# Optimization experiments

Hardware: AMD Instinct MI355X
Metric: run time of the kernel (lower is better)

## Reference

```python
import jax, jax.numpy as jnp
import numpy as np

ALPHA = 1.0  # self.a buffer (alpha=1.0 default)


def setup_inputs() -> dict:
    key = jax.random.key(0)
    k1, k2, k3 = jax.random.split(key, 3)
    B, S, DIN, DOUT = 4, 2048, 4096, 4096
    # activations and weights are int8 in [-127, 127)
    x = jax.random.randint(k1, (B, S, DIN), -127, 127, dtype=jnp.int8)
    weight = jax.random.randint(k2, (DOUT, DIN), -127, 127, dtype=jnp.int8)
    bias = jax.random.normal(k3, (1, DOUT), dtype=jnp.float32)
    return {"x": x, "weight": weight, "bias": bias}


def reference(x, weight, bias):
    # x: [B, S, DIN] int8; weight: [DOUT, DIN] int8; bias: [1, DOUT] fp32
    x_shape = x.shape
    x2 = x.reshape(-1, x_shape[-1])  # [B*S, DIN]
    y = jnp.matmul(x2, weight.T, preferred_element_type=jnp.int32)  # [B*S, DOUT] int32
    # epilogue: y + round(bias / alpha); int32 + fp32 promotes to fp32 (matches torch)
    y = y.astype(jnp.float32) + jnp.round(bias / ALPHA)
    return y.reshape(*x_shape[:-1], y.shape[-1])
```

## Files before the change

kernel.cpp:

```cpp
#include <hip/hip_runtime.h>
#include <stdint.h>
#include <math.h>


typedef int i32x4 __attribute__((ext_vector_type(4)));

static constexpr int Mdim = 8192;
static constexpr int Ndim = 4096;
static constexpr int Kdim = 4096;
static constexpr int BM = 256;
static constexpr int BN = 256;
static constexpr int BKb = 128;
static constexpr int NKT = Kdim / BKb;
static constexpr int BUF_BYTES = 65536;

typedef const __attribute__((address_space(1))) unsigned int gu32;
typedef __attribute__((address_space(3))) unsigned int lu32;

__device__ __forceinline__ void gload_lds16(const int8_t* g, char* l) {
    __builtin_amdgcn_global_load_lds((gu32*)g, (lu32*)l, 16, 0, 0);
}

__global__ void pack_i32_to_i8_both(const int* __restrict__ X32,
                                    const int* __restrict__ W32,
                                    unsigned int* __restrict__ Xp,
                                    unsigned int* __restrict__ Wp,
                                    int nX4, int nT4) {
    int idx = blockIdx.x * blockDim.x + threadIdx.x;
    int stride = gridDim.x * blockDim.x;
    for (int i = idx; i < nT4; i += stride) {
        const int* src; unsigned int* dst; int j;
        if (i < nX4) { src = X32; dst = Xp; j = i; }
        else         { src = W32; dst = Wp; j = i - nX4; }
        i32x4 v = ((const i32x4*)src)[j];
        unsigned int o = ((unsigned)v[0] & 0xffu)
                       | (((unsigned)v[1] & 0xffu) << 8)
                       | (((unsigned)v[2] & 0xffu) << 16)
                       | (((unsigned)v[3]) << 24);
        dst[j] = o;
    }
}

__global__ __launch_bounds__(512, 2) void w8a8_gemm_256(
    const int8_t* __restrict__ X, const int8_t* __restrict__ Wt,
    const float* __restrict__ bias, float* __restrict__ out)
{
    __shared__ char smem[2 * BUF_BYTES];

    const int tid = threadIdx.x;
    const int w   = tid >> 6;
    const int l   = tid & 63;
    const int fr  = l & 15;
    const int fk  = l >> 4;
    const int wm  = w >> 2;
    const int wn  = w & 3;

    const int bm = blockIdx.x * BM;
    const int bn = blockIdx.y * BN;

    const int8_t* gA = X  + (size_t)(bm + l) * Kdim + w * 16;
    const int8_t* gB = Wt + (size_t)(bn + l) * Kdim + w * 16;
    const int ldsAw = w * 2048 + l * 16;
    const int ldsBw = 32768 + w * 2048 + l * 16;

    auto stageA = [&](int t, int hm) {
        const int bufo = (t & 1) * BUF_BYTES;
        const size_t ko = (size_t)t * BKb;
#pragma unroll
        for (int s = 0; s < 2; ++s)
            gload_lds16(gA + (size_t)(hm * 128 + s * 64) * Kdim + ko,
                        &smem[bufo + hm * 16384 + s * 1024 + ldsAw]);
    };
    auto stageB = [&](int t, int hn) {
        const int bufo = (t & 1) * BUF_BYTES;
        const size_t ko = (size_t)t * BKb;
#pragma unroll
        for (int s = 0; s < 2; ++s)
            gload_lds16(gB + (size_t)(hn * 128 + s * 64) * Kdim + ko,
                        &smem[bufo + hn * 16384 + s * 1024 + ldsBw]);
    };

    const int aBase = wm * 16384 + fk * 2048 + fr * 16;
    const int bBase = 32768 + (wn >> 1) * 16384 + fk * 2048
                    + ((wn & 1) * 64 + fr) * 16;

    i32x4 acc[8][4] = {};
    i32x4 a[4][2], b[4][2];

    stageB(0, 0); stageB(0, 1); stageA(0, 0); stageA(0, 1);
    stageB(1, 0); stageB(1, 1); stageA(1, 0); stageA(1, 1);
    asm volatile("s_waitcnt vmcnt(8)" ::: "memory");
    __syncthreads();

    for (int t = 0; t < NKT; ++t) {
        const int p = (t & 1) * BUF_BYTES;

#pragma unroll
        for (int ks = 0; ks < 2; ++ks) {
#pragma unroll
            for (int j = 0; j < 4; ++j)
                a[j][ks] = *(const i32x4*)&smem[p + aBase + ks * 8192 + j * 256];
#pragma unroll
            for (int ni = 0; ni < 2; ++ni)
                b[ni][ks] = *(const i32x4*)&smem[p + bBase + ks * 8192 + ni * 256];
        }
        __builtin_amdgcn_s_barrier();
        asm volatile("s_waitcnt lgkmcnt(0)" ::: "memory");
        __builtin_amdgcn_sched_barrier(0);
        __builtin_amdgcn_s_setprio(1);
#pragma unroll
        for (int ks = 0; ks < 2; ++ks)
#pragma unroll
            for (int j = 0; j < 4; ++j)
#pragma unroll
                for (int ni = 0; ni < 2; ++ni)
                    acc[j][ni] = __builtin_amdgcn_mfma_i32_16x16x64_i8(
                        a[j][ks], b[ni][ks], acc[j][ni], 0, 0, 0);
        __builtin_amdgcn_s_setprio(0);
        __builtin_amdgcn_s_barrier();

#pragma unroll
        for (int ks = 0; ks < 2; ++ks)
#pragma unroll
            for (int ni = 2; ni < 4; ++ni)
                b[ni][ks] = *(const i32x4*)&smem[p + bBase + ks * 8192 + ni * 256];
        __builtin_amdgcn_s_barrier();
        asm volatile("s_waitcnt lgkmcnt(0)" ::: "memory");
        __builtin_amdgcn_sched_barrier(0);
        __builtin_amdgcn_s_setprio(1);
#pragma unroll
        for (int ks = 0; ks < 2; ++ks)
#pragma unroll
            for (int j = 0; j < 4; ++j)
#pragma unroll
                for (int ni = 2; ni < 4; ++ni)
                    acc[j][ni] = __builtin_amdgcn_mfma_i32_16x16x64_i8(
                        a[j][ks], b[ni][ks], acc[j][ni], 0, 0, 0);
        __builtin_amdgcn_s_setprio(0);
        __builtin_amdgcn_s_barrier();

#pragma unroll
        for (int ks = 0; ks < 2; ++ks)
#pragma unroll
            for (int j = 0; j < 4; ++j)
                a[j][ks] = *(const i32x4*)&smem[p + aBase + ks * 8192 + 1024 + j * 256];
        if (t + 2 < NKT) { stageB(t + 2, 0); stageB(t + 2, 1); }
        __builtin_amdgcn_s_barrier();
        asm volatile("s_waitcnt lgkmcnt(0)" ::: "memory");
        __builtin_amdgcn_sched_barrier(0);
        __builtin_amdgcn_s_setprio(1);
#pragma unroll
        for (int ks = 0; ks < 2; ++ks)
#pragma unroll
            for (int j = 0; j < 4; ++j)
#pragma unroll
                for (int ni = 0; ni < 2; ++ni)
                    acc[4 + j][ni] = __builtin_amdgcn_mfma_i32_16x16x64_i8(
                        a[j][ks], b[ni][ks], acc[4 + j][ni], 0, 0, 0);
        __builtin_amdgcn_s_setprio(0);
        __builtin_amdgcn_s_barrier();

        if (t + 2 < NKT) { stageA(t + 2, 0); stageA(t + 2, 1); }
        __builtin_amdgcn_sched_barrier(0);
        __builtin_amdgcn_s_setprio(1);
#pragma unroll
        for (int ks = 0; ks < 2; ++ks)
#pragma unroll
            for (int j = 0; j < 4; ++j)
#pragma unroll
                for (int ni = 2; ni < 4; ++ni)
                    acc[4 + j][ni] = __builtin_amdgcn_mfma_i32_16x16x64_i8(
                        a[j][ks], b[ni][ks], acc[4 + j][ni], 0, 0, 0);
        __builtin_amdgcn_s_setprio(0);
        if (t + 2 < NKT)      asm volatile("s_waitcnt vmcnt(8)" ::: "memory");
        else if (t + 1 < NKT) asm volatile("s_waitcnt vmcnt(0)" ::: "memory");
        __builtin_amdgcn_s_barrier();
    }

    float bv[4];
#pragma unroll
    for (int ni = 0; ni < 4; ++ni)
        bv[ni] = rintf(bias[bn + wn * 64 + ni * 16 + fr]);
#pragma unroll
    for (int mi = 0; mi < 8; ++mi) {
        const int rbase = bm + wm * 128 + mi * 16 + fk * 4;
#pragma unroll
        for (int ni = 0; ni < 4; ++ni) {
            const int col = bn + wn * 64 + ni * 16 + fr;
#pragma unroll
            for (int r = 0; r < 4; ++r)
                out[(size_t)(rbase + r) * Ndim + col] = (float)acc[mi][ni][r] + bv[ni];
        }
    }
}

extern "C" void kernel_launch(void* const* d_in, const int* in_sizes, int n_in,
                              void* d_out, int out_size, void* d_ws, size_t ws_size,
                              hipStream_t stream) {
    const int*   X32  = (const int*)d_in[0];
    const int*   W32  = (const int*)d_in[1];
    const float* bias = (const float*)d_in[2];
    float* out = (float*)d_out;

    int8_t* Xp = (int8_t*)d_ws;
    int8_t* Wp = (int8_t*)d_ws + (size_t)Mdim * Kdim;

    const int nX4 = Mdim * Kdim / 4;
    const int nW4 = Ndim * Kdim / 4;
    pack_i32_to_i8_both<<<4096, 256, 0, stream>>>(
        X32, W32, (unsigned int*)Xp, (unsigned int*)Wp, nX4, nX4 + nW4);

    dim3 grid(Mdim / BM, Ndim / BN);
    w8a8_gemm_256<<<grid, dim3(512), 0, stream>>>(Xp, Wp, bias, out);
}
```

Baseline: 432.9 us.

## Restructure K-loop into register-prefetched pipeline with staggered A/B staging

Reorganizes the main loop so LDS fragment reads for the next quadrant (and the next tile's first A/B fragments) are issued before the current MFMA block, using separate register sets per quadrant. A-tile global-to-LDS staging for tile t+1 is now issued mid-iteration instead of two tiles ahead, and the number of barriers per iteration drops from seven to two. The aim is to hide LDS latency behind MFMAs and cut synchronisation overhead. In exchange it raises register pressure, and A now has only one tile of prefetch distance, so global-load latency is less hidden.

```diff
diff --git a/kernel.cpp b/kernel.cpp
--- a/kernel.cpp
+++ b/kernel.cpp
@@ -20,6 +20,9 @@
 __device__ __forceinline__ void gload_lds16(const int8_t* g, char* l) {
     __builtin_amdgcn_global_load_lds((gu32*)g, (lu32*)l, 16, 0, 0);
 }
+
+#define LGKM0_FENCE()  do { asm volatile("s_waitcnt lgkmcnt(0)" ::: "memory"); \
+                            __builtin_amdgcn_sched_barrier(0); } while (0)
 
 __global__ void pack_i32_to_i8_both(const int* __restrict__ X32,
                                     const int* __restrict__ W32,
@@ -85,96 +88,64 @@
                     + ((wn & 1) * 64 + fr) * 16;
 
     i32x4 acc[8][4] = {};
-    i32x4 a[4][2], b[4][2];
+    i32x4 a03[4][2], a47[4][2], b01[2][2], b23[2][2];
+
+#define RD_A03(P) do { _Pragma("unroll") for (int ks = 0; ks < 2; ++ks) \
+    _Pragma("unroll") for (int j = 0; j < 4; ++j) \
+        a03[j][ks] = *(const i32x4*)&smem[(P) + aBase + ks * 8192 + j * 256]; } while (0)
+#define RD_A47(P) do { _Pragma("unroll") for (int ks = 0; ks < 2; ++ks) \
+    _Pragma("unroll") for (int j = 0; j < 4; ++j) \
+        a47[j][ks] = *(const i32x4*)&smem[(P) + aBase + ks * 8192 + 1024 + j * 256]; } while (0)
+#define RD_B01(P) do { _Pragma("unroll") for (int ks = 0; ks < 2; ++ks) \
+    _Pragma("unroll") for (int ni = 0; ni < 2; ++ni) \
+        b01[ni][ks] = *(const i32x4*)&smem[(P) + bBase + ks * 8192 + ni * 256]; } while (0)
+#define RD_B23(P) do { _Pragma("unroll") for (int ks = 0; ks < 2; ++ks) \
+    _Pragma("unroll") for (int ni = 0; ni < 2; ++ni) \
+        b23[ni][ks] = *(const i32x4*)&smem[(P) + bBase + ks * 8192 + (2 + ni) * 256]; } while (0)
+
+#define MFMA_Q(AF, BF, MO, NO) do { __builtin_amdgcn_s_setprio(1); \
+    _Pragma("unroll") for (int ks = 0; ks < 2; ++ks) \
+    _Pragma("unroll") for (int j = 0; j < 4; ++j) \
+    _Pragma("unroll") for (int ni = 0; ni < 2; ++ni) \
+        acc[(MO) + j][(NO) + ni] = __builtin_amdgcn_mfma_i32_16x16x64_i8( \
+            AF[j][ks], BF[ni][ks], acc[(MO) + j][(NO) + ni], 0, 0, 0); \
+    __builtin_amdgcn_s_setprio(0); } while (0)
 
     stageB(0, 0); stageB(0, 1); stageA(0, 0); stageA(0, 1);
-    stageB(1, 0); stageB(1, 1); stageA(1, 0); stageA(1, 1);
-    asm volatile("s_waitcnt vmcnt(8)" ::: "memory");
+    stageB(1, 0); stageB(1, 1);
+    asm volatile("s_waitcnt vmcnt(4)" ::: "memory");
     __syncthreads();
+    RD_A03(0); RD_B01(0);
 
+#pragma unroll 1
     for (int t = 0; t < NKT; ++t) {
-        const int p = (t & 1) * BUF_BYTES;
+        const int p  = (t & 1) * BUF_BYTES;
+        const int pn = ((t + 1) & 1) * BUF_BYTES;
 
-#pragma unroll
-        for (int ks = 0; ks < 2; ++ks) {
-#pragma unroll
-            for (int j = 0; j < 4; ++j)
-                a[j][ks] = *(const i32x4*)&smem[p + aBase + ks * 8192 + j * 256];
-#pragma unroll
-            for (int ni = 0; ni < 2; ++ni)
-                b[ni][ks] = *(const i32x4*)&smem[p + bBase + ks * 8192 + ni * 256];
-        }
-        __builtin_amdgcn_s_barrier();
-        asm volatile("s_waitcnt lgkmcnt(0)" ::: "memory");
+        LGKM0_FENCE();
+        RD_B23(p);
+        if (t + 1 < NKT) stageA(t + 1, 0);
         __builtin_amdgcn_sched_barrier(0);
-        __builtin_amdgcn_s_setprio(1);
-#pragma unroll
-        for (int ks = 0; ks < 2; ++ks)
-#pragma unroll
-            for (int j = 0; j < 4; ++j)
-#pragma unroll
-                for (int ni = 0; ni < 2; ++ni)
-                    acc[j][ni] = __builtin_amdgcn_mfma_i32_16x16x64_i8(
-                        a[j][ks], b[ni][ks], acc[j][ni], 0, 0, 0);
-        __builtin_amdgcn_s_setprio(0);
+        MFMA_Q(a03, b01, 0, 0);
+
+        LGKM0_FENCE();
+        RD_A47(p);
+        if (t + 1 < NKT) stageA(t + 1, 1);
+        __builtin_amdgcn_sched_barrier(0);
+        MFMA_Q(a03, b23, 0, 2);
         __builtin_amdgcn_s_barrier();
 
-#pragma unroll
-        for (int ks = 0; ks < 2; ++ks)
-#pragma unroll
-            for (int ni = 2; ni < 4; ++ni)
-                b[ni][ks] = *(const i32x4*)&smem[p + bBase + ks * 8192 + ni * 256];
-        __builtin_amdgcn_s_barrier();
-        asm volatile("s_waitcnt lgkmcnt(0)" ::: "memory");
+        LGKM0_FENCE();
+        if (t + 2 < NKT) { stageB(t + 2, 0); stageB(t + 2, 1); }
         __builtin_amdgcn_sched_barrier(0);
-        __builtin_amdgcn_s_setprio(1);
-#pragma unroll
-        for (int ks = 0; ks < 2; ++ks)
-#pragma unroll
-            for (int j = 0; j < 4; ++j)
-#pragma unroll
-                for (int ni = 2; ni < 4; ++ni)
-                    acc[j][ni] = __builtin_amdgcn_mfma_i32_16x16x64_i8(
-                        a[j][ks], b[ni][ks], acc[j][ni], 0, 0, 0);
-        __builtin_amdgcn_s_setprio(0);
+        MFMA_Q(a47, b01, 4, 0);
+        if (t + 2 < NKT)      asm volatile("s_waitcnt vmcnt(4)" ::: "memory");
+        else if (t + 1 < NKT) asm volatile("s_waitcnt vmcnt(0)" ::: "memory");
         __builtin_amdgcn_s_barrier();
 
-#pragma unroll
-        for (int ks = 0; ks < 2; ++ks)
-#pragma unroll
-            for (int j = 0; j < 4; ++j)
-                a[j][ks] = *(const i32x4*)&smem[p + aBase + ks * 8192 + 1024 + j * 256];
-        if (t + 2 < NKT) { stageB(t + 2, 0); stageB(t + 2, 1); }
-        __builtin_amdgcn_s_barrier();
-        asm volatile("s_waitcnt lgkmcnt(0)" ::: "memory");
+        if (t + 1 < NKT) { RD_A03(pn); RD_B01(pn); }
         __builtin_amdgcn_sched_barrier(0);
-        __builtin_amdgcn_s_setprio(1);
-#pragma unroll
-        for (int ks = 0; ks < 2; ++ks)
-#pragma unroll
-            for (int j = 0; j < 4; ++j)
-#pragma unroll
-                for (int ni = 0; ni < 2; ++ni)
-                    acc[4 + j][ni] = __builtin_amdgcn_mfma_i32_16x16x64_i8(
-                        a[j][ks], b[ni][ks], acc[4 + j][ni], 0, 0, 0);
-        __builtin_amdgcn_s_setprio(0);
-        __builtin_amdgcn_s_barrier();
-
-        if (t + 2 < NKT) { stageA(t + 2, 0); stageA(t + 2, 1); }
-        __builtin_amdgcn_sched_barrier(0);
-        __builtin_amdgcn_s_setprio(1);
-#pragma unroll
-        for (int ks = 0; ks < 2; ++ks)
-#pragma unroll
-            for (int j = 0; j < 4; ++j)
-#pragma unroll
-                for (int ni = 2; ni < 4; ++ni)
-                    acc[4 + j][ni] = __builtin_amdgcn_mfma_i32_16x16x64_i8(
-                        a[j][ks], b[ni][ks], acc[4 + j][ni], 0, 0, 0);
-        __builtin_amdgcn_s_setprio(0);
-        if (t + 2 < NKT)      asm volatile("s_waitcnt vmcnt(8)" ::: "memory");
-        else if (t + 1 < NKT) asm volatile("s_waitcnt vmcnt(0)" ::: "memory");
-        __builtin_amdgcn_s_barrier();
+        MFMA_Q(a47, b23, 4, 2);
     }
 
     float bv[4];
```

Result: faster. 415.1 us (-4.1%).
